# Kernel tuning notes

Hardware: AMD Instinct MI355X
Metric: run time of the kernel (lower is better)

Reference implementation:

```python
import jax, jax.numpy as jnp
import numpy as np

NUM_TILES = 64
N_EVENTS = 16777216  # routing events per update()


def setup_inputs() -> dict:
    key = jax.random.key(0)
    k1, k2 = jax.random.split(key)
    prev_tiles = jax.random.randint(k1, (N_EVENTS,), 0, NUM_TILES, dtype=jnp.int64 if jax.config.jax_enable_x64 else jnp.int32)
    curr_tiles = jax.random.randint(k2, (N_EVENTS,), 0, NUM_TILES, dtype=jnp.int64 if jax.config.jax_enable_x64 else jnp.int32)
    transitions = jnp.zeros((NUM_TILES, NUM_TILES), dtype=jnp.float32)
    total_transitions = jnp.zeros((), dtype=jnp.float32)
    return {
        "prev_tiles": prev_tiles,
        "curr_tiles": curr_tiles,
        "transitions": transitions,
        "total_transitions": total_transitions,
    }


def reference(prev_tiles, curr_tiles, transitions, total_transitions):
    """Vectorized TopologyTracker.update(): histogram of (prev, curr) pairs.

    Equivalent to: for p, c in zip(prev, curr): transitions[p, c] += 1
    """
    T = transitions.shape[0]
    # Flatten pair index into a single histogram bin id: p * T + c
    flat_idx = prev_tiles.reshape(-1) * T + curr_tiles.reshape(-1)
    counts = jax.ops.segment_sum(
        jnp.ones_like(flat_idx, dtype=transitions.dtype), flat_idx, num_segments=T * T
    ).reshape(T, T)
    new_transitions = transitions + counts
    new_total = total_transitions + jnp.asarray(prev_tiles.size, dtype=total_transitions.dtype)
    return new_transitions, new_total
```

## Files before the change

kernel.cpp:

```cpp
#include <hip/hip_runtime.h>

#define BINS 4096
#define HIST_BLOCKS 1024
#define HIST_THREADS 512
#define PAIRS 8

typedef int intx4 __attribute__((ext_vector_type(4)));

__global__ void topo_init_kernel(const float* __restrict__ transitions,
                                 const float* __restrict__ total,
                                 float* __restrict__ out,
                                 float n_events_f, int bins) {
    int i = blockIdx.x * blockDim.x + threadIdx.x;
    if (i < bins) out[i] = transitions[i];
    if (i == 0) out[bins] = total[0] + n_events_f;
}

#define CONS(Pk, Ck)                                    \
    atomicAdd(&h[(Pk.x << 6) | Ck.x], 1u);              \
    atomicAdd(&h[(Pk.y << 6) | Ck.y], 1u);              \
    atomicAdd(&h[(Pk.z << 6) | Ck.z], 1u);              \
    atomicAdd(&h[(Pk.w << 6) | Ck.w], 1u)

#define LOAD16_ASM(P0,C0,P1,C1,P2,C2,P3,C3,P4,C4,P5,C5,P6,C6,P7,C7,          \
                   o0,o1,o2,o3,o4,o5,o6,o7,pb,cb)                            \
    asm volatile(                                                            \
        "global_load_dwordx4 %[rP0], %[ro0], %[rpb]\n\t"                     \
        "global_load_dwordx4 %[rC0], %[ro0], %[rcb]\n\t"                     \
        "global_load_dwordx4 %[rP1], %[ro1], %[rpb]\n\t"                     \
        "global_load_dwordx4 %[rC1], %[ro1], %[rcb]\n\t"                     \
        "global_load_dwordx4 %[rP2], %[ro2], %[rpb]\n\t"                     \
        "global_load_dwordx4 %[rC2], %[ro2], %[rcb]\n\t"                     \
        "global_load_dwordx4 %[rP3], %[ro3], %[rpb]\n\t"                     \
        "global_load_dwordx4 %[rC3], %[ro3], %[rcb]\n\t"                     \
        "global_load_dwordx4 %[rP4], %[ro4], %[rpb]\n\t"                     \
        "global_load_dwordx4 %[rC4], %[ro4], %[rcb]\n\t"                     \
        "global_load_dwordx4 %[rP5], %[ro5], %[rpb]\n\t"                     \
        "global_load_dwordx4 %[rC5], %[ro5], %[rcb]\n\t"                     \
        "global_load_dwordx4 %[rP6], %[ro6], %[rpb]\n\t"                     \
        "global_load_dwordx4 %[rC6], %[ro6], %[rcb]\n\t"                     \
        "global_load_dwordx4 %[rP7], %[ro7], %[rpb]\n\t"                     \
        "global_load_dwordx4 %[rC7], %[ro7], %[rcb]"                         \
        : [rP0] "=&v"(P0), [rC0] "=&v"(C0), [rP1] "=&v"(P1), [rC1] "=&v"(C1),\
          [rP2] "=&v"(P2), [rC2] "=&v"(C2), [rP3] "=&v"(P3), [rC3] "=&v"(C3),\
          [rP4] "=&v"(P4), [rC4] "=&v"(C4), [rP5] "=&v"(P5), [rC5] "=&v"(C5),\
          [rP6] "=&v"(P6), [rC6] "=&v"(C6), [rP7] "=&v"(P7), [rC7] "=&v"(C7) \
        : [ro0] "v"(o0), [ro1] "v"(o1), [ro2] "v"(o2), [ro3] "v"(o3),        \
          [ro4] "v"(o4), [ro5] "v"(o5), [ro6] "v"(o6), [ro7] "v"(o7),        \
          [rpb] "s"(pb), [rcb] "s"(cb)                                       \
        : "memory")

__global__ void __launch_bounds__(HIST_THREADS)
topo_hist_kernel(const int* __restrict__ prev,
                 const int* __restrict__ curr,
                 float* __restrict__ out, int n) {
    __shared__ unsigned int h[BINS];
    for (int i = threadIdx.x; i < BINS; i += HIST_THREADS) h[i] = 0u;
    __syncthreads();

    const int n4 = n >> 2;
    const int total_threads = gridDim.x * HIST_THREADS;
    const int tid = blockIdx.x * HIST_THREADS + threadIdx.x;

    if (n4 == total_threads * PAIRS && (n & 3) == 0) {
        const int base = blockIdx.x * (HIST_THREADS * PAIRS) + threadIdx.x;
        const unsigned st = HIST_THREADS * 16u;
        const unsigned o0 = (unsigned)base * 16u;
        const unsigned o1 = o0 + st,     o2 = o0 + 2 * st, o3 = o0 + 3 * st,
                       o4 = o0 + 4 * st, o5 = o0 + 5 * st, o6 = o0 + 6 * st,
                       o7 = o0 + 7 * st;

        intx4 P0, P1, P2, P3, P4, P5, P6, P7;
        intx4 C0, C1, C2, C3, C4, C5, C6, C7;
        LOAD16_ASM(P0,C0,P1,C1,P2,C2,P3,C3,P4,C4,P5,C5,P6,C6,P7,C7,
                   o0,o1,o2,o3,o4,o5,o6,o7,prev,curr);

        asm volatile("s_waitcnt vmcnt(0)"
                     : "+v"(P0), "+v"(C0), "+v"(P1), "+v"(C1),
                       "+v"(P2), "+v"(C2), "+v"(P3), "+v"(C3),
                       "+v"(P4), "+v"(C4), "+v"(P5), "+v"(C5),
                       "+v"(P6), "+v"(C6), "+v"(P7), "+v"(C7) :: "memory");
        __syncthreads();

        CONS(P0, C0); CONS(P1, C1); CONS(P2, C2); CONS(P3, C3);
        CONS(P4, C4); CONS(P5, C5); CONS(P6, C6); CONS(P7, C7);
    } else {
        const int4* __restrict__ p4 = (const int4*)prev;
        const int4* __restrict__ c4 = (const int4*)curr;
        for (int i = tid; i < n4; i += total_threads) {
            int4 p = p4[i];
            int4 c = c4[i];
            atomicAdd(&h[(p.x << 6) | c.x], 1u);
            atomicAdd(&h[(p.y << 6) | c.y], 1u);
            atomicAdd(&h[(p.z << 6) | c.z], 1u);
            atomicAdd(&h[(p.w << 6) | c.w], 1u);
        }
        for (int t = (n4 << 2) + tid; t < n; t += total_threads) {
            atomicAdd(&h[(prev[t] << 6) | curr[t]], 1u);
        }
    }

    __syncthreads();
    for (int b = threadIdx.x; b < BINS; b += HIST_THREADS) {
        unsigned int c = h[b];
        if (c) atomicAdd(&out[b], (float)c);
    }
}

extern "C" void kernel_launch(void* const* d_in, const int* in_sizes, int n_in,
                              void* d_out, int out_size, void* d_ws, size_t ws_size,
                              hipStream_t stream) {
    const int*   prev        = (const int*)d_in[0];
    const int*   curr        = (const int*)d_in[1];
    const float* transitions = (const float*)d_in[2];
    const float* total       = (const float*)d_in[3];
    float* out = (float*)d_out;

    const int n    = in_sizes[0];
    const int bins = in_sizes[2];

    int init_blocks = (bins + 1 + 255) / 256;
    topo_init_kernel<<<init_blocks, 256, 0, stream>>>(transitions, total, out,
                                                      (float)n, bins);

    topo_hist_kernel<<<HIST_BLOCKS, HIST_THREADS, 0, stream>>>(prev, curr, out, n);
}
```

Baseline: 155.4 us.

## Use per-wave LDS histograms, staggered load waits, and smaller blocks

Gives each of the four waves in a block its own 4096-bin LDS histogram and sums them before the global flush, so waves no longer contend on the same shared counters. The single wait-all plus block barrier before consuming loads is replaced by staggered vmcnt waits, so atomics for the first pairs can start while later loads are still in flight. Blocks shrink to 256 threads and the grid doubles, keeping the per-thread work the same. LDS use grows to 64KB per block, which may reduce occupancy, and twice as many blocks issue global flush atomics.

```diff
diff --git a/kernel.cpp b/kernel.cpp
--- a/kernel.cpp
+++ b/kernel.cpp
@@ -1,9 +1,10 @@
 #include <hip/hip_runtime.h>
 
 #define BINS 4096
-#define HIST_BLOCKS 1024
-#define HIST_THREADS 512
+#define HIST_BLOCKS 2048
+#define HIST_THREADS 256
 #define PAIRS 8
+#define NWAVE (HIST_THREADS / 64)
 
 typedef int intx4 __attribute__((ext_vector_type(4)));
 
@@ -17,10 +18,14 @@
 }
 
 #define CONS(Pk, Ck)                                    \
-    atomicAdd(&h[(Pk.x << 6) | Ck.x], 1u);              \
-    atomicAdd(&h[(Pk.y << 6) | Ck.y], 1u);              \
-    atomicAdd(&h[(Pk.z << 6) | Ck.z], 1u);              \
-    atomicAdd(&h[(Pk.w << 6) | Ck.w], 1u)
+    atomicAdd(&hw[(Pk.x << 6) | Ck.x], 1u);             \
+    atomicAdd(&hw[(Pk.y << 6) | Ck.y], 1u);             \
+    atomicAdd(&hw[(Pk.z << 6) | Ck.z], 1u);             \
+    atomicAdd(&hw[(Pk.w << 6) | Ck.w], 1u)
+
+#define WAITPAIR(N, Pk, Ck)                             \
+    asm volatile("s_waitcnt vmcnt(" #N ")"              \
+                 : "+v"(Pk), "+v"(Ck)::"memory")
 
 #define LOAD16_ASM(P0,C0,P1,C1,P2,C2,P3,C3,P4,C4,P5,C5,P6,C6,P7,C7,          \
                    o0,o1,o2,o3,o4,o5,o6,o7,pb,cb)                            \
@@ -54,9 +59,15 @@
 topo_hist_kernel(const int* __restrict__ prev,
                  const int* __restrict__ curr,
                  float* __restrict__ out, int n) {
-    __shared__ unsigned int h[BINS];
-    for (int i = threadIdx.x; i < BINS; i += HIST_THREADS) h[i] = 0u;
+    __shared__ unsigned int h[NWAVE * BINS];
+    {
+        uint4* hz = (uint4*)h;
+        const uint4 z = {0u, 0u, 0u, 0u};
+        for (int i = threadIdx.x; i < (NWAVE * BINS) >> 2; i += HIST_THREADS)
+            hz[i] = z;
+    }
     __syncthreads();
+    unsigned int* hw = &h[(threadIdx.x >> 6) << 12];
 
     const int n4 = n >> 2;
     const int total_threads = gridDim.x * HIST_THREADS;
@@ -75,34 +86,33 @@
         LOAD16_ASM(P0,C0,P1,C1,P2,C2,P3,C3,P4,C4,P5,C5,P6,C6,P7,C7,
                    o0,o1,o2,o3,o4,o5,o6,o7,prev,curr);
 
-        asm volatile("s_waitcnt vmcnt(0)"
-                     : "+v"(P0), "+v"(C0), "+v"(P1), "+v"(C1),
-                       "+v"(P2), "+v"(C2), "+v"(P3), "+v"(C3),
-                       "+v"(P4), "+v"(C4), "+v"(P5), "+v"(C5),
-                       "+v"(P6), "+v"(C6), "+v"(P7), "+v"(C7) :: "memory");
-        __syncthreads();
-
-        CONS(P0, C0); CONS(P1, C1); CONS(P2, C2); CONS(P3, C3);
-        CONS(P4, C4); CONS(P5, C5); CONS(P6, C6); CONS(P7, C7);
+        WAITPAIR(14, P0, C0); CONS(P0, C0);
+        WAITPAIR(12, P1, C1); CONS(P1, C1);
+        WAITPAIR(10, P2, C2); CONS(P2, C2);
+        WAITPAIR(8,  P3, C3); CONS(P3, C3);
+        WAITPAIR(6,  P4, C4); CONS(P4, C4);
+        WAITPAIR(4,  P5, C5); CONS(P5, C5);
+        WAITPAIR(2,  P6, C6); CONS(P6, C6);
+        WAITPAIR(0,  P7, C7); CONS(P7, C7);
     } else {
         const int4* __restrict__ p4 = (const int4*)prev;
         const int4* __restrict__ c4 = (const int4*)curr;
         for (int i = tid; i < n4; i += total_threads) {
             int4 p = p4[i];
             int4 c = c4[i];
-            atomicAdd(&h[(p.x << 6) | c.x], 1u);
-            atomicAdd(&h[(p.y << 6) | c.y], 1u);
-            atomicAdd(&h[(p.z << 6) | c.z], 1u);
-            atomicAdd(&h[(p.w << 6) | c.w], 1u);
+            atomicAdd(&hw[(p.x << 6) | c.x], 1u);
+            atomicAdd(&hw[(p.y << 6) | c.y], 1u);
+            atomicAdd(&hw[(p.z << 6) | c.z], 1u);
+            atomicAdd(&hw[(p.w << 6) | c.w], 1u);
         }
         for (int t = (n4 << 2) + tid; t < n; t += total_threads) {
-            atomicAdd(&h[(prev[t] << 6) | curr[t]], 1u);
+            atomicAdd(&hw[(prev[t] << 6) | curr[t]], 1u);
         }
     }
 
     __syncthreads();
     for (int b = threadIdx.x; b < BINS; b += HIST_THREADS) {
-        unsigned int c = h[b];
+        unsigned int c = h[b] + h[b + BINS] + h[b + 2 * BINS] + h[b + 3 * BINS];
         if (c) atomicAdd(&out[b], (float)c);
     }
 }
```

Measured after the change: 173.9 us. +11.9%, slower.
